# Kernel tuning notes

Measured on AMD Instinct MI355X. Metric: run time of the kernel, lower is better.

## Reference

```python
import math
import jax, jax.numpy as jnp
import numpy as np

NUM_BUCKETS = 32
MAX_DISTANCE = 128
B, T, E, H, D = 2, 2048, 1024, 16, 64
INIT_SCALE = 0.1


def _relative_position_bucket(rel, num_buckets=NUM_BUCKETS, max_distance=MAX_DISTANCE):
    # T5-style bucketing; rel is int [T, T]
    nb = num_buckets // 2
    buckets = (rel > 0).astype(jnp.int32) * nb
    rel_abs = jnp.abs(rel)
    max_exact = nb // 2
    is_small = rel_abs < max_exact
    # guard log(0); those positions are selected by is_small anyway
    val_large = max_exact + (
        jnp.log(jnp.maximum(rel_abs, 1).astype(jnp.float32) / max_exact)
        / math.log(max_distance / max_exact) * (nb - max_exact)
    ).astype(jnp.int32)
    val_large = jnp.minimum(val_large, nb - 1)
    return buckets + jnp.where(is_small, rel_abs, val_large)


def setup_inputs() -> dict:
    key = jax.random.key(0)
    ks = jax.random.split(key, 6)
    x = jax.random.normal(ks[0], (B, T, E), dtype=jnp.float32)
    # nn.Linear weights are [out_features, in_features], init normal(std=0.1)
    Wq = jax.random.normal(ks[1], (H * D, E), dtype=jnp.float32) * INIT_SCALE
    Wk = jax.random.normal(ks[2], (H * D, E), dtype=jnp.float32) * INIT_SCALE
    Wv = jax.random.normal(ks[3], (H * D, E), dtype=jnp.float32) * INIT_SCALE
    Wo = jax.random.normal(ks[4], (E, H * D), dtype=jnp.float32) * INIT_SCALE
    # nn.Embedding default init: standard normal
    rel_emb = jax.random.normal(ks[5], (NUM_BUCKETS, H), dtype=jnp.float32)
    return {"x": x, "Wq": Wq, "Wk": Wk, "Wv": Wv, "Wo": Wo, "rel_emb": rel_emb}


def reference(x, Wq, Wk, Wv, Wo, rel_emb):
    b, t, _ = x.shape
    scale = D ** (-0.5)
    q = jnp.einsum('bte,fe->btf', x, Wq).reshape(b, t, H, D).transpose(0, 2, 1, 3)
    k = jnp.einsum('bte,fe->btf', x, Wk).reshape(b, t, H, D).transpose(0, 2, 1, 3)
    v = jnp.einsum('bte,fe->btf', x, Wv).reshape(b, t, H, D).transpose(0, 2, 1, 3)
    attn = jnp.einsum('bhtd,bhsd->bhts', q, k) * scale  # [B,H,T,T]
    # T5 relative position bias
    pos = jnp.arange(t)
    rel = pos[:, None] - pos[None, :]
    buckets = _relative_position_bucket(rel)
    bias = rel_emb[buckets]                    # [T,T,H]
    attn = attn + bias.transpose(2, 0, 1)[None]  # [1,H,T,T]
    # causal mask (triu, diagonal=1)
    causal = jnp.triu(jnp.ones((t, t), dtype=bool), k=1)
    attn = jnp.where(causal[None, None], -jnp.inf, attn)
    attn = jax.nn.softmax(attn, axis=-1)
    out = jnp.einsum('bhts,bhsd->bhtd', attn, v).transpose(0, 2, 1, 3).reshape(b, t, H * D)
    return jnp.einsum('btf,ef->bte', out, Wo)
```

## Files before the change

kernel.cpp:

```cpp
#include <hip/hip_runtime.h>
#include <hip/hip_bf16.h>
#include <stdint.h>


typedef __attribute__((ext_vector_type(8))) short bf16x8;
typedef __attribute__((ext_vector_type(4))) float f32x4;

#define MFMA16(a, b, c) __builtin_amdgcn_mfma_f32_16x16x32_bf16((a), (b), (c), 0, 0, 0)

typedef __attribute__((address_space(1))) void gvoid_t;
typedef __attribute__((address_space(3))) void lvoid_t;

__device__ __forceinline__ void gload16(const void* g, void* l) {
    __builtin_amdgcn_global_load_lds((gvoid_t*)g, (lvoid_t*)l, 16, 0, 0);
}

__device__ __forceinline__ ushort f2bf_rne(float f) {
    union { float f; uint32_t u; } v; v.f = f;
    uint32_t u = v.u;
    return (ushort)((u + 0x7FFFu + ((u >> 16) & 1u)) >> 16);
}

__global__ void cvt_all(const float* __restrict__ x,
                        const float* __restrict__ wq, const float* __restrict__ wk,
                        const float* __restrict__ wv, const float* __restrict__ wo,
                        ushort* __restrict__ out) {
    int i = (blockIdx.x * 256 + threadIdx.x) * 4;
    int sel = i >> 20;
    const float* src; int off;
    if (sel < 4) { src = x; off = i; }
    else {
        src = (sel == 4) ? wq : (sel == 5) ? wk : (sel == 6) ? wv : wo;
        off = i & 1048575;
    }
    float4 f = *(const float4*)(src + off);
    ushort4 o;
    o.x = f2bf_rne(f.x); o.y = f2bf_rne(f.y);
    o.z = f2bf_rne(f.z); o.w = f2bf_rne(f.w);
    *(ushort4*)(out + i) = o;
}

__global__ void build_bias(const float* __restrict__ rel_emb, float* __restrict__ bias_tab) {
    int idx = blockIdx.x * 256 + threadIdx.x;
    int h = idx >> 11, rel = idx & 2047;
    int bucket;
    if (rel == 0) bucket = 0;
    else if (rel < 8) bucket = 16 + rel;
    else {
        int t;
        if      (rel >= 91) t = 7;
        else if (rel >= 64) t = 6;
        else if (rel >= 46) t = 5;
        else if (rel >= 32) t = 4;
        else if (rel >= 23) t = 3;
        else if (rel >= 16) t = 2;
        else if (rel >= 12) t = 1;
        else                t = 0;
        bucket = 24 + t;
    }
    bias_tab[idx] = rel_emb[bucket * 16 + h];
}

template<int MODE>
__global__ __launch_bounds__(256, MODE == 0 ? 3 : 2) void gemm_bt(
    const ushort* __restrict__ A,
    const ushort* __restrict__ W0, const ushort* __restrict__ W1, const ushort* __restrict__ W2,
    ushort* __restrict__ outq, ushort* __restrict__ outk, ushort* __restrict__ outvt,
    float* __restrict__ outf)
{
    constexpr int BM  = (MODE == 0) ? 128 : 64;
    constexpr int ACH = BM / 32;
    constexpr int MI  = (MODE == 0) ? 4 : 2;
    __shared__ __align__(16) ushort lsA[BM * 64];
    __shared__ __align__(16) ushort lsB[128 * 64];
    const int tid = threadIdx.x;
    const int lane = tid & 63, w = tid >> 6;
    const int g = lane >> 4, c16 = lane & 15;
    const int m0 = blockIdx.x * BM;
    const int wm = w >> 1, wn = w & 1;

    const ushort* W;
    int n0, widx = 0;
    if (MODE == 0) {
        widx = blockIdx.y >> 3;
        W = (widx == 0) ? W0 : (widx == 1) ? W1 : W2;
        n0 = (blockIdx.y & 7) * 128;
    } else {
        W = W0;
        n0 = blockIdx.y * 128;
    }

    f32x4 acc[MI][4];
    #pragma unroll
    for (int i = 0; i < MI; i++)
        #pragma unroll
        for (int j = 0; j < 4; j++) acc[i][j] = (f32x4){0.f, 0.f, 0.f, 0.f};

    int acrow[ACH], acj[ACH], bcrow[4], bcj[4];
    #pragma unroll
    for (int i = 0; i < ACH; i++) {
        int c = (i * 4 + w) * 64 + lane;
        acrow[i] = c >> 3; acj[i] = (c & 7) ^ (acrow[i] & 7);
    }
    #pragma unroll
    for (int i = 0; i < 4; i++) {
        int c = (i * 4 + w) * 64 + lane;
        bcrow[i] = c >> 3; bcj[i] = (c & 7) ^ (bcrow[i] & 7);
    }

    for (int kt = 0; kt < 1024; kt += 64) {
        __syncthreads();
        #pragma unroll
        for (int i = 0; i < ACH; i++)
            gload16(A + (size_t)(m0 + acrow[i]) * 1024 + kt + acj[i] * 8,
                    lsA + (i * 4 + w) * 512);
        #pragma unroll
        for (int i = 0; i < 4; i++)
            gload16(W + (size_t)(n0 + bcrow[i]) * 1024 + kt + bcj[i] * 8,
                    lsB + (i * 4 + w) * 512);
        __syncthreads();
        #pragma unroll
        for (int kk = 0; kk < 2; kk++) {
            bf16x8 af[MI], bfv[4];
            #pragma unroll
            for (int mi = 0; mi < MI; mi++) {
                int row = wm * (16 * MI) + mi * 16 + c16;
                af[mi] = *(const bf16x8*)(lsA + row * 64 + (((kk * 4 + g) ^ (row & 7)) * 8));
            }
            #pragma unroll
            for (int ni = 0; ni < 4; ni++) {
                int row = wn * 64 + ni * 16 + c16;
                bfv[ni] = *(const bf16x8*)(lsB + row * 64 + (((kk * 4 + g) ^ (row & 7)) * 8));
            }
            #pragma unroll
            for (int mi = 0; mi < MI; mi++)
                #pragma unroll
                for (int ni = 0; ni < 4; ni++)
                    acc[mi][ni] = MFMA16(af[mi], bfv[ni], acc[mi][ni]);
        }
    }

    const float qs = (MODE == 0 && widx == 0) ? 0.125f : 1.0f;
    #pragma unroll
    for (int mi = 0; mi < MI; mi++) {
        #pragma unroll
        for (int ni = 0; ni < 4; ni++) {
            int mg = m0 + wm * (16 * MI) + mi * 16 + g * 4;
            if (MODE == 0) {
                int f = n0 + wn * 64 + ni * 16 + c16;
                int h = f >> 6, d = f & 63;
                if (widx < 2) {
                    ushort* dst = (widx == 0) ? outq : outk;
                    #pragma unroll
                    for (int r = 0; r < 4; r++) {
                        int m = mg + r, b = m >> 11, t = m & 2047;
                        dst[((b * 16 + h) * 2048 + t) * 64 + d] = f2bf_rne(acc[mi][ni][r] * qs);
                    }
                } else {
                    int b = mg >> 11, t = mg & 2047;
                    ushort4 pk;
                    pk.x = f2bf_rne(acc[mi][ni][0]); pk.y = f2bf_rne(acc[mi][ni][1]);
                    pk.z = f2bf_rne(acc[mi][ni][2]); pk.w = f2bf_rne(acc[mi][ni][3]);
                    *(ushort4*)(outvt + ((size_t)(b * 16 + h) * 64 + d) * 2048 + t) = pk;
                }
            } else {
                int ng = n0 + wn * 64 + ni * 16 + c16;
                #pragma unroll
                for (int r = 0; r < 4; r++) {
                    int m = mg + r;
                    outf[(size_t)m * 1024 + ng] = acc[mi][ni][r];
                }
            }
        }
    }
}

__global__ __launch_bounds__(256, 4) void attn_kernel(
    const ushort* __restrict__ qb_, const ushort* __restrict__ kb_,
    const ushort* __restrict__ vtb, const float* __restrict__ bias_tab,
    ushort* __restrict__ ob)
{
    __shared__ __align__(16) ushort Ks[64 * 64];
    __shared__ __align__(16) ushort Vs[64 * 64];
    __shared__ __align__(16) ushort Ps[4][16 * 72];

    const int tid = threadIdx.x, lane = tid & 63, w = tid >> 6;
    const int g = lane >> 4, c16 = lane & 15;
    const int p = blockIdx.x;
    const int xcd = p & 7, j = p >> 3;
    const int round = j >> 5, px = j & 31;
    const int bh = (xcd << 2) | round;
    const int qb = (round & 1) ? (31 - px) : px;
    const int b = bh >> 4, h = bh & 15;

    const ushort* qh = qb_ + (size_t)bh * 2048 * 64;
    const ushort* kh = kb_ + (size_t)bh * 2048 * 64;
    const ushort* vh = vtb + (size_t)bh * 64 * 2048;
    const float* bt = bias_tab + h * 2048;
    const float bias_far = bt[128];
    const int q0 = qb * 64;
    const int qrow = q0 + w * 16 + c16;

    int crow[2], cj[2];
    #pragma unroll
    for (int i = 0; i < 2; i++) {
        int c = (i * 4 + w) * 64 + lane;
        crow[i] = c >> 3;
        cj[i] = (c & 7) ^ (crow[i] & 7);
    }

    bf16x8 qf[2];
    #pragma unroll
    for (int kk = 0; kk < 2; kk++)
        qf[kk] = *(const bf16x8*)(qh + (size_t)qrow * 64 + kk * 32 + g * 8);

    float m_run = -1e30f, l_run = 0.f;
    f32x4 o[4];
    #pragma unroll
    for (int ni = 0; ni < 4; ni++) o[ni] = (f32x4){0.f, 0.f, 0.f, 0.f};

    for (int j64 = 0; j64 <= qb; j64++) {
        const int k0 = j64 * 64;
        __syncthreads();
        #pragma unroll
        for (int i = 0; i < 2; i++) {
            gload16(kh + (size_t)(k0 + crow[i]) * 64 + cj[i] * 8, Ks + (i * 4 + w) * 512);
            gload16(vh + (size_t)crow[i] * 2048 + k0 + cj[i] * 8, Vs + (i * 4 + w) * 512);
        }
        __syncthreads();

        f32x4 s[4];
        #pragma unroll
        for (int f = 0; f < 4; f++) s[f] = (f32x4){0.f, 0.f, 0.f, 0.f};
        __builtin_amdgcn_s_setprio(1);
        #pragma unroll
        for (int kk = 0; kk < 2; kk++) {
            #pragma unroll
            for (int f = 0; f < 4; f++) {
                int row = f * 16 + c16;
                bf16x8 a = *(const bf16x8*)(Ks + row * 64 + (((kk * 4 + g) ^ (row & 7)) * 8));
                s[f] = MFMA16(a, qf[kk], s[f]);
            }
        }
        __builtin_amdgcn_s_setprio(0);

        const bool near = (qb - j64) < 3;
        const bool diag = (j64 == qb);
        float p4[4][4];
        float m_new, lt = 0.f;
        if (near) {
            float mt = -1e30f;
            #pragma unroll
            for (int f = 0; f < 4; f++)
                #pragma unroll
                for (int r = 0; r < 4; r++) {
                    int kpos = k0 + f * 16 + g * 4 + r;
                    int rel = qrow - kpos;
                    float lg;
                    if (diag && rel < 0) lg = -1e30f;
                    else lg = s[f][r] + bt[rel];
                    p4[f][r] = lg;
                    mt = fmaxf(mt, lg);
                }
            mt = fmaxf(mt, __shfl_xor(mt, 16));
            mt = fmaxf(mt, __shfl_xor(mt, 32));
            m_new = fmaxf(m_run, mt);
            #pragma unroll
            for (int f = 0; f < 4; f++)
                #pragma unroll
                for (int r = 0; r < 4; r++) {
                    float e = __expf(p4[f][r] - m_new);
                    p4[f][r] = e;
                    lt += e;
                }
        } else {
            float mt = -1e30f;
            #pragma unroll
            for (int f = 0; f < 4; f++)
                #pragma unroll
                for (int r = 0; r < 4; r++) mt = fmaxf(mt, s[f][r]);
            mt = fmaxf(mt, __shfl_xor(mt, 16));
            mt = fmaxf(mt, __shfl_xor(mt, 32));
            m_new = fmaxf(m_run, mt + bias_far);
            float madj = m_new - bias_far;
            #pragma unroll
            for (int f = 0; f < 4; f++)
                #pragma unroll
                for (int r = 0; r < 4; r++) {
                    float e = __expf(s[f][r] - madj);
                    p4[f][r] = e;
                    lt += e;
                }
        }
        lt += __shfl_xor(lt, 16);
        lt += __shfl_xor(lt, 32);
        float alpha = __expf(m_run - m_new);
        l_run = l_run * alpha + lt;
        m_run = m_new;
        #pragma unroll
        for (int ni = 0; ni < 4; ni++) {
            o[ni][0] *= alpha; o[ni][1] *= alpha; o[ni][2] *= alpha; o[ni][3] *= alpha;
        }

        #pragma unroll
        for (int f = 0; f < 4; f++) {
            ushort4 pk;
            pk.x = f2bf_rne(p4[f][0]); pk.y = f2bf_rne(p4[f][1]);
            pk.z = f2bf_rne(p4[f][2]); pk.w = f2bf_rne(p4[f][3]);
            *(ushort4*)(&Ps[w][c16 * 72 + f * 16 + g * 4]) = pk;
        }
        __builtin_amdgcn_s_setprio(1);
        #pragma unroll
        for (int kk = 0; kk < 2; kk++) {
            bf16x8 pf = *(const bf16x8*)(&Ps[w][c16 * 72 + kk * 32 + g * 8]);
            #pragma unroll
            for (int ni = 0; ni < 4; ni++) {
                int row = ni * 16 + c16;
                bf16x8 av = *(const bf16x8*)(Vs + row * 64 + (((kk * 4 + g) ^ (row & 7)) * 8));
                o[ni] = MFMA16(av, pf, o[ni]);
            }
        }
        __builtin_amdgcn_s_setprio(0);
    }

    float inv = 1.f / l_run;
    size_t base = ((size_t)(b * 2048 + qrow)) * 1024 + h * 64;
    #pragma unroll
    for (int ni = 0; ni < 4; ni++) {
        ushort4 pk;
        pk.x = f2bf_rne(o[ni][0] * inv); pk.y = f2bf_rne(o[ni][1] * inv);
        pk.z = f2bf_rne(o[ni][2] * inv); pk.w = f2bf_rne(o[ni][3] * inv);
        *(ushort4*)(ob + base + ni * 16 + g * 4) = pk;
    }
}

extern "C" void kernel_launch(void* const* d_in, const int* in_sizes, int n_in,
                              void* d_out, int out_size, void* d_ws, size_t ws_size,
                              hipStream_t stream) {
    const float* x       = (const float*)d_in[0];
    const float* Wq      = (const float*)d_in[1];
    const float* Wk      = (const float*)d_in[2];
    const float* Wv      = (const float*)d_in[3];
    const float* Wo      = (const float*)d_in[4];
    const float* rel_emb = (const float*)d_in[5];

    char* ws = (char*)d_ws;
    ushort* xbf = (ushort*)(ws);
    ushort* wqb = (ushort*)(ws + (8u  << 20));
    ushort* wkb = (ushort*)(ws + (10u << 20));
    ushort* wvb = (ushort*)(ws + (12u << 20));
    ushort* wob = (ushort*)(ws + (14u << 20));
    ushort* qbf = (ushort*)(ws + (16u << 20));
    ushort* kbf = (ushort*)(ws + (24u << 20));
    ushort* vtb = (ushort*)(ws + (32u << 20));
    ushort* obf = (ushort*)(ws + (40u << 20));
    float*  btab = (float*)(ws + (48u << 20));

    cvt_all<<<8192, 256, 0, stream>>>(x, Wq, Wk, Wv, Wo, xbf);
    build_bias<<<128, 256, 0, stream>>>(rel_emb, btab);

    gemm_bt<0><<<dim3(32, 24), 256, 0, stream>>>(xbf, wqb, wkb, wvb, qbf, kbf, vtb, nullptr);
    attn_kernel<<<1024, 256, 0, stream>>>(qbf, kbf, vtb, btab, obf);
    gemm_bt<1><<<dim3(64, 8), 256, 0, stream>>>(obf, wob, nullptr, nullptr,
                                                nullptr, nullptr, nullptr, (float*)d_out);
}
```

Before: 179.4 us.

## Double-buffer GEMM LDS tiles with K=32 stages and vmcnt-based prefetch

New measurement: 181.3 us. About the same (+1.1%).

```diff
diff --git a/kernel.cpp b/kernel.cpp
--- a/kernel.cpp
+++ b/kernel.cpp
@@ -68,11 +68,11 @@
     ushort* __restrict__ outq, ushort* __restrict__ outk, ushort* __restrict__ outvt,
     float* __restrict__ outf)
 {
-    constexpr int BM  = (MODE == 0) ? 128 : 64;
-    constexpr int ACH = BM / 32;
-    constexpr int MI  = (MODE == 0) ? 4 : 2;
-    __shared__ __align__(16) ushort lsA[BM * 64];
-    __shared__ __align__(16) ushort lsB[128 * 64];
+    constexpr int BM = (MODE == 0) ? 128 : 64;
+    constexpr int AG = BM / 64;
+    constexpr int MI = (MODE == 0) ? 4 : 2;
+    __shared__ __align__(16) ushort lsA[2][BM * 32];
+    __shared__ __align__(16) ushort lsB[2][128 * 32];
     const int tid = threadIdx.x;
     const int lane = tid & 63, w = tid >> 6;
     const int g = lane >> 4, c16 = lane & 15;
@@ -96,49 +96,62 @@
         #pragma unroll
         for (int j = 0; j < 4; j++) acc[i][j] = (f32x4){0.f, 0.f, 0.f, 0.f};
 
-    int acrow[ACH], acj[ACH], bcrow[4], bcj[4];
-    #pragma unroll
-    for (int i = 0; i < ACH; i++) {
+    int acrow[AG], acj[AG], bcrow[2], bcj[2];
+    #pragma unroll
+    for (int i = 0; i < AG; i++) {
         int c = (i * 4 + w) * 64 + lane;
-        acrow[i] = c >> 3; acj[i] = (c & 7) ^ (acrow[i] & 7);
-    }
-    #pragma unroll
-    for (int i = 0; i < 4; i++) {
+        acrow[i] = c >> 2; acj[i] = (c & 3) ^ ((acrow[i] >> 1) & 3);
+    }
+    #pragma unroll
+    for (int i = 0; i < 2; i++) {
         int c = (i * 4 + w) * 64 + lane;
-        bcrow[i] = c >> 3; bcj[i] = (c & 7) ^ (bcrow[i] & 7);
-    }
-
-    for (int kt = 0; kt < 1024; kt += 64) {
-        __syncthreads();
-        #pragma unroll
-        for (int i = 0; i < ACH; i++)
+        bcrow[i] = c >> 2; bcj[i] = (c & 3) ^ ((bcrow[i] >> 1) & 3);
+    }
+
+    auto stage = [&](int buf, int kt) {
+        #pragma unroll
+        for (int i = 0; i < AG; i++)
             gload16(A + (size_t)(m0 + acrow[i]) * 1024 + kt + acj[i] * 8,
-                    lsA + (i * 4 + w) * 512);
-        #pragma unroll
-        for (int i = 0; i < 4; i++)
+                    &lsA[buf][(i * 4 + w) * 512]);
+        #pragma unroll
+        for (int i = 0; i < 2; i++)
             gload16(W + (size_t)(n0 + bcrow[i]) * 1024 + kt + bcj[i] * 8,
-                    lsB + (i * 4 + w) * 512);
-        __syncthreads();
-        #pragma unroll
-        for (int kk = 0; kk < 2; kk++) {
-            bf16x8 af[MI], bfv[4];
-            #pragma unroll
-            for (int mi = 0; mi < MI; mi++) {
-                int row = wm * (16 * MI) + mi * 16 + c16;
-                af[mi] = *(const bf16x8*)(lsA + row * 64 + (((kk * 4 + g) ^ (row & 7)) * 8));
-            }
-            #pragma unroll
-            for (int ni = 0; ni < 4; ni++) {
-                int row = wn * 64 + ni * 16 + c16;
-                bfv[ni] = *(const bf16x8*)(lsB + row * 64 + (((kk * 4 + g) ^ (row & 7)) * 8));
-            }
-            #pragma unroll
-            for (int mi = 0; mi < MI; mi++)
-                #pragma unroll
-                for (int ni = 0; ni < 4; ni++)
-                    acc[mi][ni] = MFMA16(af[mi], bfv[ni], acc[mi][ni]);
-        }
-    }
+                    &lsB[buf][(i * 4 + w) * 512]);
+    };
+
+    auto compute = [&](int cur) {
+        bf16x8 af[MI], bfv[4];
+        #pragma unroll
+        for (int mi = 0; mi < MI; mi++) {
+            int row = wm * (16 * MI) + mi * 16 + c16;
+            af[mi] = *(const bf16x8*)(&lsA[cur][row * 32 + ((g ^ ((row >> 1) & 3)) * 8)]);
+        }
+        #pragma unroll
+        for (int ni = 0; ni < 4; ni++) {
+            int row = wn * 64 + ni * 16 + c16;
+            bfv[ni] = *(const bf16x8*)(&lsB[cur][row * 32 + ((g ^ ((row >> 1) & 3)) * 8)]);
+        }
+        #pragma unroll
+        for (int mi = 0; mi < MI; mi++)
+            #pragma unroll
+            for (int ni = 0; ni < 4; ni++)
+                acc[mi][ni] = MFMA16(af[mi], bfv[ni], acc[mi][ni]);
+    };
+
+    stage(0, 0);
+    stage(1, 32);
+    for (int t = 0; t < 31; ++t) {
+        if constexpr (MODE == 0) asm volatile("s_waitcnt vmcnt(4)" ::: "memory");
+        else                     asm volatile("s_waitcnt vmcnt(3)" ::: "memory");
+        __builtin_amdgcn_s_barrier();
+        const int cur = t & 1;
+        compute(cur);
+        __builtin_amdgcn_s_barrier();
+        if (t < 30) stage(cur, (t + 2) * 32);
+    }
+    asm volatile("s_waitcnt vmcnt(0)" ::: "memory");
+    __builtin_amdgcn_s_barrier();
+    compute(1);
 
     const float qs = (MODE == 0 && widx == 0) ? 0.125f : 1.0f;
     #pragma unroll
```
